# Kernel tuning notes

Measured on AMD Instinct MI355X. Metric: run time of the kernel, lower is better.

## Reference

```python
import jax, jax.numpy as jnp
import numpy as np

N_NODES, N_EDGES, D_IN, D_OUT = 40000, 640000, 128, 128


def setup_inputs() -> dict:
    key = jax.random.key(0)
    k0, k1, k2, k3, k4 = jax.random.split(key, 5)
    x = jax.random.normal(k0, (N_NODES, D_IN), dtype=jnp.float32)
    src = jax.random.randint(k1, (N_EDGES,), 0, N_NODES)
    dst = jax.random.randint(k2, (N_EDGES,), 0, N_NODES)
    edge_weight = jax.random.uniform(k3, (N_EDGES,), dtype=jnp.float32)
    # GraphConv learned parameters (Glorot-ish init) and bias
    W = jax.random.normal(k4, (D_IN, D_OUT), dtype=jnp.float32) * (1.0 / np.sqrt(D_IN))
    b = jnp.zeros((D_OUT,), dtype=jnp.float32)
    return {"x": x, "src": src, "dst": dst, "edge_weight": edge_weight, "W": W, "b": b}


def reference(x, src, dst, edge_weight, W, b):
    N = x.shape[0]
    # EdgeWeightNorm(norm='right') on all-ones edge weights: w_e = 1 / in_degree(dst_e)
    deg = jax.ops.segment_sum(jnp.ones_like(edge_weight), dst, num_segments=N)  # [N]
    inv_deg = jnp.where(deg > 0, 1.0 / deg, 0.0)  # allow_zero_in_degree
    w = inv_deg[dst] * edge_weight  # norm_weight *= self.edge_weight  [E]
    # GraphConv norm='none' with edge_weight: h[v] = sum_{e:(u->v)} w_e * x[u]
    msg = x[src] * w[:, None]  # [E, D_IN]
    h = jax.ops.segment_sum(msg, dst, num_segments=N)  # [N, D_IN]
    return h @ W + b  # [N, D_OUT]
```

## Files before the change

kernel.cpp:

```cpp
#include <hip/hip_runtime.h>

#define N_NODES 40000
#define N_EDGES 640000
#define D 128
#define NB 157


__global__ __launch_bounds__(256) void init_kernel(int* __restrict__ deg,
                                                   int* __restrict__ cursor) {
    int i = blockIdx.x * 256 + threadIdx.x;
    if (i < N_NODES) { deg[i] = 0; cursor[i] = 0; }
}

__global__ __launch_bounds__(256) void degree_kernel(const int* __restrict__ dst,
                                                     int* __restrict__ deg) {
    int e = blockIdx.x * 256 + threadIdx.x;
    if (e < N_EDGES) atomicAdd(&deg[dst[e]], 1);
}

__global__ __launch_bounds__(256) void reduce_kernel(const int* __restrict__ deg,
                                                     int* __restrict__ bsum) {
    __shared__ int s[256];
    int t = threadIdx.x;
    int idx = blockIdx.x * 256 + t;
    s[t] = (idx < N_NODES) ? deg[idx] : 0;
    __syncthreads();
#pragma unroll
    for (int off = 128; off > 0; off >>= 1) {
        if (t < off) s[t] += s[t + off];
        __syncthreads();
    }
    if (t == 0) bsum[blockIdx.x] = s[0];
}

__global__ __launch_bounds__(256) void scanb_kernel(int* __restrict__ bsum) {
    __shared__ int s[256];
    int t = threadIdx.x;
    int v = (t < NB) ? bsum[t] : 0;
    s[t] = v;
    __syncthreads();
#pragma unroll
    for (int off = 1; off < 256; off <<= 1) {
        int u = (t >= off) ? s[t - off] : 0;
        __syncthreads();
        s[t] += u;
        __syncthreads();
    }
    if (t < NB) bsum[t] = s[t] - v;
}

__global__ __launch_bounds__(256) void offs_kernel(const int* __restrict__ deg,
                                                   const int* __restrict__ bsum,
                                                   int* __restrict__ offs,
                                                   float* __restrict__ invdeg) {
    __shared__ int s[256];
    int t = threadIdx.x;
    int idx = blockIdx.x * 256 + t;
    int d = (idx < N_NODES) ? deg[idx] : 0;
    s[t] = d;
    __syncthreads();
#pragma unroll
    for (int off = 1; off < 256; off <<= 1) {
        int u = (t >= off) ? s[t - off] : 0;
        __syncthreads();
        s[t] += u;
        __syncthreads();
    }
    int excl = s[t] - d + bsum[blockIdx.x];
    if (idx < N_NODES) {
        offs[idx] = excl;
        invdeg[idx] = (d > 0) ? (1.0f / (float)d) : 0.0f;
        if (idx == N_NODES - 1) offs[N_NODES] = excl + d;
    }
}

__global__ __launch_bounds__(256) void bucket_kernel(const int* __restrict__ src,
                                                     const int* __restrict__ dst,
                                                     const float* __restrict__ ew,
                                                     const float* __restrict__ invdeg,
                                                     const int* __restrict__ offs,
                                                     int* __restrict__ cursor,
                                                     int* __restrict__ es,
                                                     float* __restrict__ ews) {
    int e = blockIdx.x * 256 + threadIdx.x;
    if (e >= N_EDGES) return;
    int d = dst[e];
    int pos = offs[d] + atomicAdd(&cursor[d], 1);
    es[pos] = src[e];
    ews[pos] = ew[e] * invdeg[d];
}

__global__ __launch_bounds__(256) void gemm_xw_kernel(const float* __restrict__ x,
                                                      const float* __restrict__ W,
                                                      float* __restrict__ y) {
    __shared__ float Ws[D * D];
    __shared__ float xs[16 * D];
    const int tid = threadIdx.x;
    const int rowbase = blockIdx.x * 16;

    float4* Ws4 = reinterpret_cast<float4*>(Ws);
    const float4* W4 = reinterpret_cast<const float4*>(W);
#pragma unroll
    for (int i = 0; i < 16; ++i)
        Ws4[tid + i * 256] = W4[tid + i * 256];

    float4* xs4 = reinterpret_cast<float4*>(xs);
    const float4* x4 = reinterpret_cast<const float4*>(x) + rowbase * (D / 4);
    xs4[tid]       = x4[tid];
    xs4[tid + 256] = x4[tid + 256];
    __syncthreads();

    const int lane = tid & 31;
    const int rp   = tid >> 5;
    const float* xrow0 = xs + (rp * 2) * D;
    const float* xrow1 = xrow0 + D;

    float4 acc0 = {0.f, 0.f, 0.f, 0.f};
    float4 acc1 = {0.f, 0.f, 0.f, 0.f};
#pragma unroll 4
    for (int k = 0; k < D; ++k) {
        float4 wv = Ws4[k * (D / 4) + lane];
        float xa = xrow0[k];
        float xb = xrow1[k];
        acc0.x += xa * wv.x; acc0.y += xa * wv.y; acc0.z += xa * wv.z; acc0.w += xa * wv.w;
        acc1.x += xb * wv.x; acc1.y += xb * wv.y; acc1.z += xb * wv.z; acc1.w += xb * wv.w;
    }

    float4* y4 = reinterpret_cast<float4*>(y);
    int r0 = rowbase + rp * 2;
    y4[r0 * (D / 4) + lane]       = acc0;
    y4[(r0 + 1) * (D / 4) + lane] = acc1;
}

__global__ __launch_bounds__(256) void gather_kernel(const int* __restrict__ offs,
                                                     const int* __restrict__ es,
                                                     const float* __restrict__ ews,
                                                     const float* __restrict__ y,
                                                     const float* __restrict__ b,
                                                     float* __restrict__ out) {
    int gid = blockIdx.x * 256 + threadIdx.x;
    int v    = gid >> 5;
    int part = gid & 31;
    if (v >= N_NODES) return;
    int beg = offs[v];
    int end = offs[v + 1];
    const float4* y4 = reinterpret_cast<const float4*>(y);
    float4 acc = {0.f, 0.f, 0.f, 0.f};
    for (int base = beg; base < end; base += 32) {
        int n = end - base; if (n > 32) n = 32;
        int   se = 0;
        float we = 0.0f;
        if (part < n) { se = es[base + part]; we = ews[base + part]; }
        for (int j = 0; j < n; ++j) {
            int   s = __shfl(se, j, 32);
            float w = __shfl(we, j, 32);
            float4 t = y4[s * (D / 4) + part];
            acc.x += w * t.x; acc.y += w * t.y; acc.z += w * t.z; acc.w += w * t.w;
        }
    }
    float4 bv = reinterpret_cast<const float4*>(b)[part];
    acc.x += bv.x; acc.y += bv.y; acc.z += bv.z; acc.w += bv.w;
    reinterpret_cast<float4*>(out)[v * (D / 4) + part] = acc;
}

extern "C" void kernel_launch(void* const* d_in, const int* in_sizes, int n_in,
                              void* d_out, int out_size, void* d_ws, size_t ws_size,
                              hipStream_t stream) {
    const float* x   = (const float*)d_in[0];
    const int*   src = (const int*)d_in[1];
    const int*   dst = (const int*)d_in[2];
    const float* ew  = (const float*)d_in[3];
    const float* W   = (const float*)d_in[4];
    const float* b   = (const float*)d_in[5];
    float* out = (float*)d_out;

    char* ws = (char*)d_ws;
    float* y      = (float*)ws;                       ws += (size_t)N_NODES * D * 4;
    int*   deg    = (int*)ws;                         ws += (size_t)N_NODES * 4;
    int*   cursor = (int*)ws;                         ws += (size_t)N_NODES * 4;
    float* invdeg = (float*)ws;                       ws += (size_t)N_NODES * 4;
    int*   offs   = (int*)ws;                         ws += (size_t)(N_NODES + 16) * 4;
    int*   bsum   = (int*)ws;                         ws += (size_t)((NB + 16) & ~3) * 4;
    int*   es     = (int*)ws;                         ws += (size_t)N_EDGES * 4;
    float* ews    = (float*)ws;

    init_kernel<<<(N_NODES + 255) / 256, 256, 0, stream>>>(deg, cursor);
    degree_kernel<<<(N_EDGES + 255) / 256, 256, 0, stream>>>(dst, deg);
    reduce_kernel<<<NB, 256, 0, stream>>>(deg, bsum);
    scanb_kernel<<<1, 256, 0, stream>>>(bsum);
    offs_kernel<<<NB, 256, 0, stream>>>(deg, bsum, offs, invdeg);
    gemm_xw_kernel<<<N_NODES / 16, 256, 0, stream>>>(x, W, y);
    bucket_kernel<<<(N_EDGES + 255) / 256, 256, 0, stream>>>(src, dst, ew, invdeg,
                                                             offs, cursor, es, ews);
    {
        long long total = (long long)N_NODES * 32;
        gather_kernel<<<(int)((total + 255) / 256), 256, 0, stream>>>(offs, es, ews, y, b, out);
    }
}
```

Measured before the change: 223.3 us.

## Fuse block scan into offsets, pack edge pairs, defer degree normalization

Removes the single-block scan kernel by having each offsets block reduce preceding block sums itself. Edge source and raw weight are packed into one int2 array so the bucket and gather kernels do a single 8-byte access per edge. The inverse-degree multiply moves to the end of the gather, and the projection GEMM computes four rows per thread. This trades a small amount of redundant reduction work for one fewer launch and fewer memory transactions.

```diff
diff --git a/kernel.cpp b/kernel.cpp
--- a/kernel.cpp
+++ b/kernel.cpp
@@ -4,6 +4,7 @@
 #define N_EDGES 640000
 #define D 128
 #define NB 157
+#define GEMM_ROWS 32
 
 
 __global__ __launch_bounds__(256) void init_kernel(int* __restrict__ deg,
@@ -33,28 +34,27 @@
     if (t == 0) bsum[blockIdx.x] = s[0];
 }
 
-__global__ __launch_bounds__(256) void scanb_kernel(int* __restrict__ bsum) {
-    __shared__ int s[256];
-    int t = threadIdx.x;
-    int v = (t < NB) ? bsum[t] : 0;
-    s[t] = v;
-    __syncthreads();
-#pragma unroll
-    for (int off = 1; off < 256; off <<= 1) {
-        int u = (t >= off) ? s[t - off] : 0;
-        __syncthreads();
-        s[t] += u;
-        __syncthreads();
-    }
-    if (t < NB) bsum[t] = s[t] - v;
-}
-
 __global__ __launch_bounds__(256) void offs_kernel(const int* __restrict__ deg,
                                                    const int* __restrict__ bsum,
                                                    int* __restrict__ offs,
                                                    float* __restrict__ invdeg) {
     __shared__ int s[256];
+    __shared__ int base_s;
     int t = threadIdx.x;
+
+    int v = (t < blockIdx.x && t < NB) ? bsum[t] : 0;
+    s[t] = v;
+    __syncthreads();
+#pragma unroll
+    for (int off = 128; off > 0; off >>= 1) {
+        if (t < off) s[t] += s[t + off];
+        __syncthreads();
+    }
+    if (t == 0) base_s = s[0];
+    __syncthreads();
+    int base = base_s;
+    __syncthreads();
+
     int idx = blockIdx.x * 256 + t;
     int d = (idx < N_NODES) ? deg[idx] : 0;
     s[t] = d;
@@ -66,7 +66,7 @@
         s[t] += u;
         __syncthreads();
     }
-    int excl = s[t] - d + bsum[blockIdx.x];
+    int excl = s[t] - d + base;
     if (idx < N_NODES) {
         offs[idx] = excl;
         invdeg[idx] = (d > 0) ? (1.0f / (float)d) : 0.0f;
@@ -77,26 +77,23 @@
 __global__ __launch_bounds__(256) void bucket_kernel(const int* __restrict__ src,
                                                      const int* __restrict__ dst,
                                                      const float* __restrict__ ew,
-                                                     const float* __restrict__ invdeg,
                                                      const int* __restrict__ offs,
                                                      int* __restrict__ cursor,
-                                                     int* __restrict__ es,
-                                                     float* __restrict__ ews) {
+                                                     int2* __restrict__ pairs) {
     int e = blockIdx.x * 256 + threadIdx.x;
     if (e >= N_EDGES) return;
     int d = dst[e];
     int pos = offs[d] + atomicAdd(&cursor[d], 1);
-    es[pos] = src[e];
-    ews[pos] = ew[e] * invdeg[d];
+    pairs[pos] = make_int2(src[e], __float_as_int(ew[e]));
 }
 
 __global__ __launch_bounds__(256) void gemm_xw_kernel(const float* __restrict__ x,
                                                       const float* __restrict__ W,
                                                       float* __restrict__ y) {
     __shared__ float Ws[D * D];
-    __shared__ float xs[16 * D];
+    __shared__ float xs[GEMM_ROWS * D];
     const int tid = threadIdx.x;
-    const int rowbase = blockIdx.x * 16;
+    const int rowbase = blockIdx.x * GEMM_ROWS;
 
     float4* Ws4 = reinterpret_cast<float4*>(Ws);
     const float4* W4 = reinterpret_cast<const float4*>(W);
@@ -106,35 +103,40 @@
 
     float4* xs4 = reinterpret_cast<float4*>(xs);
     const float4* x4 = reinterpret_cast<const float4*>(x) + rowbase * (D / 4);
-    xs4[tid]       = x4[tid];
-    xs4[tid + 256] = x4[tid + 256];
+#pragma unroll
+    for (int i = 0; i < GEMM_ROWS * (D / 4) / 256; ++i)
+        xs4[tid + i * 256] = x4[tid + i * 256];
     __syncthreads();
 
     const int lane = tid & 31;
     const int rp   = tid >> 5;
-    const float* xrow0 = xs + (rp * 2) * D;
-    const float* xrow1 = xrow0 + D;
-
-    float4 acc0 = {0.f, 0.f, 0.f, 0.f};
-    float4 acc1 = {0.f, 0.f, 0.f, 0.f};
+    const float* xr0 = xs + (rp * 4 + 0) * D;
+    const float* xr1 = xs + (rp * 4 + 1) * D;
+    const float* xr2 = xs + (rp * 4 + 2) * D;
+    const float* xr3 = xs + (rp * 4 + 3) * D;
+
+    float4 a0 = {0.f,0.f,0.f,0.f}, a1 = a0, a2 = a0, a3 = a0;
 #pragma unroll 4
     for (int k = 0; k < D; ++k) {
         float4 wv = Ws4[k * (D / 4) + lane];
-        float xa = xrow0[k];
-        float xb = xrow1[k];
-        acc0.x += xa * wv.x; acc0.y += xa * wv.y; acc0.z += xa * wv.z; acc0.w += xa * wv.w;
-        acc1.x += xb * wv.x; acc1.y += xb * wv.y; acc1.z += xb * wv.z; acc1.w += xb * wv.w;
+        float x0 = xr0[k], x1 = xr1[k], x2 = xr2[k], x3 = xr3[k];
+        a0.x += x0*wv.x; a0.y += x0*wv.y; a0.z += x0*wv.z; a0.w += x0*wv.w;
+        a1.x += x1*wv.x; a1.y += x1*wv.y; a1.z += x1*wv.z; a1.w += x1*wv.w;
+        a2.x += x2*wv.x; a2.y += x2*wv.y; a2.z += x2*wv.z; a2.w += x2*wv.w;
+        a3.x += x3*wv.x; a3.y += x3*wv.y; a3.z += x3*wv.z; a3.w += x3*wv.w;
     }
 
     float4* y4 = reinterpret_cast<float4*>(y);
-    int r0 = rowbase + rp * 2;
-    y4[r0 * (D / 4) + lane]       = acc0;
-    y4[(r0 + 1) * (D / 4) + lane] = acc1;
+    int r0 = rowbase + rp * 4;
+    y4[(r0 + 0) * (D / 4) + lane] = a0;
+    y4[(r0 + 1) * (D / 4) + lane] = a1;
+    y4[(r0 + 2) * (D / 4) + lane] = a2;
+    y4[(r0 + 3) * (D / 4) + lane] = a3;
 }
 
 __global__ __launch_bounds__(256) void gather_kernel(const int* __restrict__ offs,
-                                                     const int* __restrict__ es,
-                                                     const float* __restrict__ ews,
+                                                     const int2* __restrict__ pairs,
+                                                     const float* __restrict__ invdeg,
                                                      const float* __restrict__ y,
                                                      const float* __restrict__ b,
                                                      float* __restrict__ out) {
@@ -148,18 +150,21 @@
     float4 acc = {0.f, 0.f, 0.f, 0.f};
     for (int base = beg; base < end; base += 32) {
         int n = end - base; if (n > 32) n = 32;
-        int   se = 0;
-        float we = 0.0f;
-        if (part < n) { se = es[base + part]; we = ews[base + part]; }
+        int2 pe = make_int2(0, 0);
+        if (part < n) pe = pairs[base + part];
         for (int j = 0; j < n; ++j) {
-            int   s = __shfl(se, j, 32);
-            float w = __shfl(we, j, 32);
+            int   s = __shfl(pe.x, j, 32);
+            float w = __int_as_float(__shfl(pe.y, j, 32));
             float4 t = y4[s * (D / 4) + part];
             acc.x += w * t.x; acc.y += w * t.y; acc.z += w * t.z; acc.w += w * t.w;
         }
     }
+    float idv = invdeg[v];
     float4 bv = reinterpret_cast<const float4*>(b)[part];
-    acc.x += bv.x; acc.y += bv.y; acc.z += bv.z; acc.w += bv.w;
+    acc.x = acc.x * idv + bv.x;
+    acc.y = acc.y * idv + bv.y;
+    acc.z = acc.z * idv + bv.z;
+    acc.w = acc.w * idv + bv.w;
     reinterpret_cast<float4*>(out)[v * (D / 4) + part] = acc;
 }
 
@@ -180,20 +185,18 @@
     int*   cursor = (int*)ws;                         ws += (size_t)N_NODES * 4;
     float* invdeg = (float*)ws;                       ws += (size_t)N_NODES * 4;
     int*   offs   = (int*)ws;                         ws += (size_t)(N_NODES + 16) * 4;
-    int*   bsum   = (int*)ws;                         ws += (size_t)((NB + 16) & ~3) * 4;
-    int*   es     = (int*)ws;                         ws += (size_t)N_EDGES * 4;
-    float* ews    = (float*)ws;
+    int*   bsum   = (int*)ws;                         ws += (size_t)((NB + 19) & ~3) * 4;
+    int2*  pairs  = (int2*)ws;
 
     init_kernel<<<(N_NODES + 255) / 256, 256, 0, stream>>>(deg, cursor);
     degree_kernel<<<(N_EDGES + 255) / 256, 256, 0, stream>>>(dst, deg);
     reduce_kernel<<<NB, 256, 0, stream>>>(deg, bsum);
-    scanb_kernel<<<1, 256, 0, stream>>>(bsum);
     offs_kernel<<<NB, 256, 0, stream>>>(deg, bsum, offs, invdeg);
-    gemm_xw_kernel<<<N_NODES / 16, 256, 0, stream>>>(x, W, y);
-    bucket_kernel<<<(N_EDGES + 255) / 256, 256, 0, stream>>>(src, dst, ew, invdeg,
-                                                             offs, cursor, es, ews);
+    gemm_xw_kernel<<<N_NODES / GEMM_ROWS, 256, 0, stream>>>(x, W, y);
+    bucket_kernel<<<(N_EDGES + 255) / 256, 256, 0, stream>>>(src, dst, ew,
+                                                             offs, cursor, pairs);
     {
         long long total = (long long)N_NODES * 32;
-        gather_kernel<<<(int)((total + 255) / 256), 256, 0, stream>>>(offs, es, ews, y, b, out);
-    }
-}
+        gather_kernel<<<(int)((total + 255) / 256), 256, 0, stream>>>(offs, pairs, invdeg, y, b, out);
+    }
+}
```

New measurement: 212.1 us. -5.0%, faster.
